# Performance work log

Measured on AMD Instinct MI355X. Metric: run time of the kernel, lower is better.

Reference implementation:

```python
import jax, jax.numpy as jnp
import numpy as np

PATCHES = [(4, 4), (2, 2)]  # (width, height) per stream chunk
SCALE = 2
DM = 256


def conv2d(x, w, bias, pad=0):
    y = jax.lax.conv_general_dilated(
        x, w, window_strides=(1, 1), padding=[(pad, pad), (pad, pad)],
        dimension_numbers=("NCHW", "OIHW", "NCHW"))
    return y + bias[None, :, None, None]


def to_patches(x, b, t, dk, out_h, ph, out_w, pw):
    # x: [b*t, dk, out_h*ph, out_w*pw] -> [b, t*out_h*out_w, dk*ph*pw]
    x = x.reshape(b, t, dk, out_h, ph, out_w, pw)
    return x.transpose(0, 1, 3, 5, 2, 4, 6).reshape(b, t * out_h * out_w, dk * ph * pw)


def from_patches(y, b, t, dk, out_h, ph, out_w, pw):
    # y: [b, t*out_h*out_w, dk*ph*pw] -> [b*t, dk, out_h*ph, out_w*pw]
    y = y.reshape(b, t, out_h, out_w, dk, ph, pw)
    return y.transpose(0, 1, 4, 2, 5, 3, 6).reshape(b * t, dk, out_h * ph, out_w * pw)


def attention(q, k, v):
    d = q.shape[-1]
    scores = jnp.einsum("bnd,bmd->bnm", q, k) / jnp.sqrt(jnp.asarray(d, q.dtype))
    p = jax.nn.softmax(scores, axis=-1)
    return jnp.einsum("bnm,bmd->bnd", p, v)


def forward(x_lo, x_hi, b,
            wq_lo, bq_lo, wk_lo, bk_lo, wv_lo, bv_lo,
            wq_hi, bq_hi, wk_hi, bk_hi, wv_hi, bv_hi,
            wo_lo, bo_lo, wo_hi, bo_hi):
    bt_lo, _, h, w = x_lo.shape
    bt_hi, _, h_, w_ = x_hi.shape
    t_lo = bt_lo // b
    t_hi = bt_hi // b
    n_p = len(PATCHES)
    d_k_lo = DM * SCALE ** 2 // n_p
    d_k_hi = DM // n_p

    q_lo_all = conv2d(x_lo, wq_lo, bq_lo)
    k_lo_all = conv2d(x_lo, wk_lo, bk_lo)
    v_lo_all = conv2d(x_lo, wv_lo, bv_lo)
    q_hi_all = conv2d(x_hi, wq_hi, bq_hi)
    k_hi_all = conv2d(x_hi, wk_hi, bk_hi)
    v_hi_all = conv2d(x_hi, wv_hi, bv_hi)

    outs_lo, outs_hi = [], []
    for i, (width, height) in enumerate(PATCHES):
        out_w, out_h = w // width, h // height
        sl_lo = slice(i * d_k_lo, (i + 1) * d_k_lo)
        sl_hi = slice(i * d_k_hi, (i + 1) * d_k_hi)
        ql = to_patches(q_lo_all[:, sl_lo], b, t_lo, d_k_lo, out_h, height, out_w, width)
        kl = to_patches(k_lo_all[:, sl_lo], b, t_lo, d_k_lo, out_h, height, out_w, width)
        vl = to_patches(v_lo_all[:, sl_lo], b, t_lo, d_k_lo, out_h, height, out_w, width)
        qh = to_patches(q_hi_all[:, sl_hi], b, t_hi, d_k_hi, out_h, height * SCALE, out_w, width * SCALE)
        kh = to_patches(k_hi_all[:, sl_hi], b, t_hi, d_k_hi, out_h, height * SCALE, out_w, width * SCALE)
        vh = to_patches(v_hi_all[:, sl_hi], b, t_hi, d_k_hi, out_h, height * SCALE, out_w, width * SCALE)

        q = jnp.concatenate([ql, qh], axis=1)
        k = jnp.concatenate([kl, kh], axis=1)
        v = jnp.concatenate([vl, vh], axis=1)
        y = attention(q, k, v)

        n_lo = t_lo * out_h * out_w
        y_lo = from_patches(y[:, :n_lo], b, t_lo, d_k_lo, out_h, height, out_w, width)
        y_hi = from_patches(y[:, n_lo:], b, t_hi, d_k_hi, out_h, height * SCALE, out_w, width * SCALE)
        outs_lo.append(y_lo)
        outs_hi.append(y_hi)

    out_lo = jnp.concatenate(outs_lo, axis=1)
    out_hi = jnp.concatenate(outs_hi, axis=1)
    out_lo = jax.nn.leaky_relu(conv2d(out_lo, wo_lo, bo_lo, pad=1), 0.2)
    out_hi = jax.nn.leaky_relu(conv2d(out_hi, wo_hi, bo_hi, pad=1), 0.2)
    return out_lo, out_hi


def setup_inputs() -> dict:
    key = jax.random.key(0)
    ks = jax.random.split(key, 12)
    dm2 = DM * SCALE ** 2  # 1024
    s = 0.02
    inp = {
        "x_lo": jax.random.normal(ks[0], (16, DM, 32, 32), jnp.float32),
        "x_hi": jax.random.normal(ks[1], (16, DM, 64, 64), jnp.float32),
        "b": 4,
        "wq_lo": jax.random.normal(ks[2], (dm2, DM, 1, 1), jnp.float32) * s,
        "bq_lo": jnp.zeros((dm2,), jnp.float32),
        "wk_lo": jax.random.normal(ks[3], (dm2, DM, 1, 1), jnp.float32) * s,
        "bk_lo": jnp.zeros((dm2,), jnp.float32),
        "wv_lo": jax.random.normal(ks[4], (dm2, DM, 1, 1), jnp.float32) * s,
        "bv_lo": jnp.zeros((dm2,), jnp.float32),
        "wq_hi": jax.random.normal(ks[5], (DM, DM, 1, 1), jnp.float32) * s,
        "bq_hi": jnp.zeros((DM,), jnp.float32),
        "wk_hi": jax.random.normal(ks[6], (DM, DM, 1, 1), jnp.float32) * s,
        "bk_hi": jnp.zeros((DM,), jnp.float32),
        "wv_hi": jax.random.normal(ks[7], (DM, DM, 1, 1), jnp.float32) * s,
        "bv_hi": jnp.zeros((DM,), jnp.float32),
        "wo_lo": jax.random.normal(ks[8], (DM, dm2, 3, 3), jnp.float32) * s,
        "bo_lo": jnp.zeros((DM,), jnp.float32),
        "wo_hi": jax.random.normal(ks[9], (DM, DM, 3, 3), jnp.float32) * s,
        "bo_hi": jnp.zeros((DM,), jnp.float32),
    }
    return inp


def reference(x_lo, x_hi, b,
              wq_lo, bq_lo, wk_lo, bk_lo, wv_lo, bv_lo,
              wq_hi, bq_hi, wk_hi, bk_hi, wv_hi, bv_hi,
              wo_lo, bo_lo, wo_hi, bo_hi):
    return forward(x_lo, x_hi, b,
                   wq_lo, bq_lo, wk_lo, bk_lo, wv_lo, bv_lo,
                   wq_hi, bq_hi, wk_hi, bk_hi, wv_hi, bv_hi,
                   wo_lo, bo_lo, wo_hi, bo_hi)
```

## Files before the change

kernel.cpp:

```cpp
#include <hip/hip_runtime.h>
#include <hip/hip_bf16.h>
#include <stdint.h>

typedef __attribute__((ext_vector_type(8))) short short8;
typedef __attribute__((ext_vector_type(4))) short short4v;
typedef __attribute__((ext_vector_type(2))) short short2v;
typedef __attribute__((ext_vector_type(4))) float floatx4;

__device__ __forceinline__ unsigned short f2b(float f) {
  unsigned u = __builtin_bit_cast(unsigned, f);
  unsigned r = u + 0x7fffu + ((u >> 16) & 1u);
  return (unsigned short)(r >> 16);
}
__device__ __forceinline__ float b2f(unsigned short h) {
  unsigned u = ((unsigned)h) << 16;
  return __builtin_bit_cast(float, u);
}
__device__ __forceinline__ void glds16(const unsigned short* src, unsigned short* dst) {
  __builtin_amdgcn_global_load_lds((const __attribute__((address_space(1))) void*)src,
                                   (__attribute__((address_space(3))) void*)dst, 16, 0, 0);
}
__device__ __forceinline__ int swz(int r, int o) {
  return (r << 9) + (o ^ ((((o >> 7) & 3) ^ (r & 7)) << 4));
}

struct GemmP {
  const unsigned short* A;
  const unsigned short* B;
  long sAb, sBb;
  int lda, ldb, K;
  unsigned short* C; long sCb; int ldc;
  float* Cp;
  const float* bias;
  unsigned short *Q0, *K0, *V0t, *Q1, *K1, *V1t;
};

template<int EPI>
__global__ __launch_bounds__(512) void gemm256(GemmP p) {
  __shared__ __align__(16) unsigned short LDS[65536];
  const int tid = threadIdx.x;
  const int wv = tid >> 6, lane = tid & 63;
  const int wm = wv >> 2, wn = wv & 3;
  const int g = lane >> 4, l16 = lane & 15;
  const int bz = blockIdx.z;
  const int m0 = blockIdx.y * 256, n0 = blockIdx.x * 256;

  int bb = bz, koff = 0, Keff = p.K;
  if constexpr (EPI == 1) { bb = bz >> 3; koff = (bz & 7) * (p.K >> 3); Keff = p.K >> 3; }
  const unsigned short* Ab = p.A + (long)bb * p.sAb + (long)m0 * p.lda + koff;
  const unsigned short* Bb = p.B + (long)bb * p.sBb + (long)n0 * p.ldb + koff;
  const int NT = Keff >> 5;

  const int r0 = tid >> 2;
  const int cs = (tid & 3) ^ ((r0 >> 1) & 3);
  const unsigned short* aS0 = Ab + (long)r0 * p.lda + cs * 8;
  const unsigned short* aS1 = aS0 + (long)128 * p.lda;
  const unsigned short* bS0 = Bb + (long)r0 * p.ldb + cs * 8;
  const unsigned short* bS1 = bS0 + (long)128 * p.ldb;
  unsigned short* const lds0 = (unsigned short*)LDS;
  const int wbase = wv * 512;

  auto STAGE_A = [&](int t) {
    unsigned short* d = lds0 + (t & 3) * 16384;
    const long ko = (long)t * 32;
    glds16(aS0 + ko, d + wbase);
    glds16(aS1 + ko, d + 4096 + wbase);
  };
  auto STAGE_B = [&](int t) {
    unsigned short* d = lds0 + (t & 3) * 16384 + 8192;
    const long ko = (long)t * 32;
    glds16(bS0 + ko, d + wbase);
    glds16(bS1 + ko, d + 4096 + wbase);
  };

  STAGE_A(0); STAGE_B(0); STAGE_A(1); STAGE_B(1); STAGE_A(2); STAGE_B(2);

  floatx4 acc[8][4];
  const floatx4 z4 = {0.f, 0.f, 0.f, 0.f};
#pragma unroll
  for (int i = 0; i < 8; ++i)
#pragma unroll
    for (int j = 0; j < 4; ++j) acc[i][j] = z4;

  const int loff = l16 * 32 + ((g ^ ((l16 >> 1) & 3)) * 8);
  const int aRowB = wm * 128;

  for (int t = 0; t < NT; ++t) {
    const unsigned short* As = lds0 + (t & 3) * 16384;
    const unsigned short* Bs = As + 8192;
    if (t < NT - 2)        asm volatile("s_waitcnt vmcnt(8)" ::: "memory");
    else if (t == NT - 2)  asm volatile("s_waitcnt vmcnt(4)" ::: "memory");
    else                   asm volatile("s_waitcnt vmcnt(0)" ::: "memory");
    __builtin_amdgcn_s_barrier();
    __builtin_amdgcn_sched_barrier(0);
    if (t + 3 < NT) STAGE_A(t + 3);
    short8 bf[4], af[4], ag[4];
#pragma unroll
    for (int ni = 0; ni < 4; ++ni)
      bf[ni] = *(const short8*)(Bs + (wn * 64 + ni * 16) * 32 + loff);
#pragma unroll
    for (int mi = 0; mi < 4; ++mi)
      af[mi] = *(const short8*)(As + (aRowB + mi * 16) * 32 + loff);
#pragma unroll
    for (int mi = 0; mi < 4; ++mi)
      ag[mi] = *(const short8*)(As + (aRowB + 64 + mi * 16) * 32 + loff);
    __builtin_amdgcn_s_setprio(1);
#pragma unroll
    for (int mi = 0; mi < 4; ++mi)
#pragma unroll
      for (int ni = 0; ni < 4; ++ni)
        acc[mi][ni] = __builtin_amdgcn_mfma_f32_16x16x32_bf16(af[mi], bf[ni], acc[mi][ni], 0, 0, 0);
    __builtin_amdgcn_s_setprio(0);
    if (t + 3 < NT) STAGE_B(t + 3);
    __builtin_amdgcn_s_setprio(1);
#pragma unroll
    for (int mi = 0; mi < 4; ++mi)
#pragma unroll
      for (int ni = 0; ni < 4; ++ni)
        acc[4 + mi][ni] = __builtin_amdgcn_mfma_f32_16x16x32_bf16(ag[mi], bf[ni], acc[4 + mi][ni], 0, 0, 0);
    __builtin_amdgcn_s_setprio(0);
  }

  if constexpr (EPI == 1) {
    float* C = p.Cp + (long)bz * p.sCb;
#pragma unroll
    for (int mi = 0; mi < 8; ++mi) {
#pragma unroll
      for (int ni = 0; ni < 4; ++ni) {
        const int col = n0 + wn * 64 + ni * 16 + l16;
#pragma unroll
        for (int r4 = 0; r4 < 4; ++r4) {
          const int row = m0 + wm * 128 + mi * 16 + g * 4 + r4;
          C[(long)row * p.ldc + col] = acc[mi][ni][r4];
        }
      }
    }
  } else {
    __syncthreads();
    char* shb = (char*)LDS;
    const int sel = (EPI == 2) ? (m0 >> 10) : (m0 >> 8);
#pragma unroll
    for (int mi = 0; mi < 8; ++mi) {
#pragma unroll
      for (int ni = 0; ni < 4; ++ni) {
        const int c = wn * 64 + ni * 16 + l16;
#pragma unroll
        for (int r4 = 0; r4 < 4; ++r4) {
          const int rr = wm * 128 + mi * 16 + g * 4 + r4;
          float v = acc[mi][ni][r4];
          if constexpr (EPI == 2 || EPI == 3) {
            v += p.bias[m0 + rr];
            if (sel == 0) {
              float sc;
              if constexpr (EPI == 2) sc = ((m0 & 1023) < 512) ? 0.011048543456039806f
                                                               : 0.02209708691207961f;
              else                    sc = (rr < 128) ? 0.011048543456039806f
                                                      : 0.02209708691207961f;
              v *= sc;
            }
          }
          *(unsigned short*)(shb + swz(rr, c * 2)) = f2b(v);
        }
      }
    }
    __syncthreads();

    if constexpr (EPI == 0) {
      unsigned short* C = p.C + (long)bz * p.sCb;
#pragma unroll
      for (int j = 0; j < 16; ++j) {
        const int e = j * 512 + tid;
        const int r = e >> 5, ck = e & 31;
        short8 v = *(const short8*)(shb + swz(r, ck * 16));
        *(short8*)(C + (long)(m0 + r) * p.ldc + n0 + ck * 8) = v;
      }
    } else if constexpr (EPI == 2) {
      const int chb = m0 & 1023;
      const bool cfg0 = chb < 512;
      const int b = bz >> 2, tt = bz & 3;
      const int k0 = n0 >> 8;
      unsigned short* dst = cfg0 ? (sel == 0 ? p.Q0 : sel == 1 ? p.K0 : p.V0t)
                                 : (sel == 0 ? p.Q1 : sel == 1 ? p.K1 : p.V1t);
      if (sel != 2) {
        if (cfg0) {
          const long base = (long)(b * 512) * 8192;
#pragma unroll
          for (int j = 0; j < 16; ++j) {
            const int e = j * 512 + tid;
            const int pi = e >> 9, idx2 = e & 511;
            const int ch = idx2 >> 1, hf = idx2 & 1;
            const int oyL = pi >> 3, ox = pi & 7;
            const int nseq = (tt * 8 + 2 * k0 + oyL) * 8 + ox;
            const int yl = oyL * 4 + hf * 2;
            short4v a = *(const short4v*)(shb + swz(ch, (yl * 32 + ox * 4) * 2));
            short4v b2 = *(const short4v*)(shb + swz(ch, ((yl + 1) * 32 + ox * 4) * 2));
            short8 v = {a[0], a[1], a[2], a[3], b2[0], b2[1], b2[2], b2[3]};
            *(short8*)(dst + base + (long)nseq * 8192 + (chb + ch) * 16 + hf * 8) = v;
          }
        } else {
          const int c2lo = chb - 512;
          const long base = (long)(b * 2048) * 2048;
#pragma unroll
          for (int j = 0; j < 16; ++j) {
            const int e = j * 512 + tid;
            const int pi = e >> 7, cp = e & 127;
            const int oyL = pi >> 4, ox = pi & 15;
            const int nseq = (tt * 16 + 4 * k0 + oyL) * 16 + ox;
            short8 v;
#pragma unroll
            for (int rr = 0; rr < 2; ++rr) {
#pragma unroll
              for (int k = 0; k < 2; ++k) {
                short2v pr = *(const short2v*)(shb +
                    swz(cp * 2 + rr, ((oyL * 2 + k) * 32 + ox * 2) * 2));
                v[rr * 4 + k * 2] = pr[0];
                v[rr * 4 + k * 2 + 1] = pr[1];
              }
            }
            *(short8*)(dst + base + (long)nseq * 2048 + (c2lo + cp * 2) * 4) = v;
          }
        }
      } else {
        if (cfg0) {
          const long base = (long)(b * 8192) * 512;
#pragma unroll
          for (int j = 0; j < 16; ++j) {
            const int e = j * 512 + tid;
            const int oyL = e >> 12, fu = e & 4095;
            const int ch = fu >> 4, pp = fu & 15;
            const int py = pp >> 2, px = pp & 3;
            const int yl = oyL * 4 + py;
            short8 v;
#pragma unroll
            for (int ox = 0; ox < 8; ++ox)
              v[ox] = *(const unsigned short*)(shb + swz(ch, (yl * 32 + ox * 4 + px) * 2));
            const long f = (long)(chb + ch) * 16 + pp;
            *(short8*)(dst + base + f * 512 + (tt * 8 + 2 * k0 + oyL) * 8) = v;
          }
        } else {
          const int c2lo = chb - 512;
          const long base = (long)(b * 2048) * 2048;
#pragma unroll
          for (int j = 0; j < 16; ++j) {
            const int e = j * 512 + tid;
            const int he = e & 1, oyL = (e >> 1) & 3, fu = e >> 3;
            const int c2 = fu >> 2, pp = fu & 3;
            const int py = pp >> 1, px = pp & 1;
            const int yl = oyL * 2 + py;
            short8 v;
#pragma unroll
            for (int i = 0; i < 8; ++i) {
              const int ox = he * 8 + i;
              v[i] = *(const unsigned short*)(shb + swz(c2, (yl * 32 + ox * 2 + px) * 2));
            }
            const long f = (long)(c2lo + c2) * 4 + pp;
            *(short8*)(dst + base + f * 2048 + (tt * 16 + 4 * k0 + oyL) * 16 + he * 8) = v;
          }
        }
      }
    } else if constexpr (EPI == 3) {
      const int b = bz >> 2, tt = bz & 3;
      const int k0 = n0 >> 8;
      const int oyA = k0 >> 1, pyb = (k0 & 1) * 4;
      unsigned short* dstA = sel == 0 ? p.Q0 : sel == 1 ? p.K0 : p.V0t;
      unsigned short* dstB = sel == 0 ? p.Q1 : sel == 1 ? p.K1 : p.V1t;
      if (sel != 2) {
#pragma unroll
        for (int j = 0; j < 16; ++j) {
          const int e = j * 512 + tid;
          if (e < 4096) {
            const int ox = e >> 9, cy = e & 511;
            const int ch = cy >> 2, yl = cy & 3;
            const int nseq = 256 + (tt * 8 + oyA) * 8 + ox;
            short8 v = *(const short8*)(shb + swz(ch, (yl * 64 + ox * 8) * 2));
            *(short8*)(dstA + ((long)(b * 512 + nseq)) * 8192 + ch * 64 + (pyb + yl) * 8) = v;
          } else {
            const int ee = e - 4096;
            const int ox = ee >> 8, cc = ee & 255;
            const int c2 = cc >> 1, hf = cc & 1;
            const int nseq = 1024 + (tt * 16 + k0) * 16 + ox;
            short8 v;
#pragma unroll
            for (int k = 0; k < 2; ++k) {
              short4v a = *(const short4v*)(shb +
                  swz(128 + c2, ((hf * 2 + k) * 64 + ox * 4) * 2));
              v[k * 4] = a[0]; v[k * 4 + 1] = a[1]; v[k * 4 + 2] = a[2]; v[k * 4 + 3] = a[3];
            }
            *(short8*)(dstB + ((long)(b * 2048 + nseq)) * 2048 + c2 * 16 + hf * 8) = v;
          }
        }
      } else {
#pragma unroll
        for (int j = 0; j < 16; ++j) {
          const int e = j * 512 + tid;
          if (e < 4096) {
            const int ch = e >> 5, yl = (e >> 3) & 3, px = e & 7;
            short8 v;
#pragma unroll
            for (int ox = 0; ox < 8; ++ox)
              v[ox] = *(const unsigned short*)(shb + swz(ch, (yl * 64 + ox * 8 + px) * 2));
            const long f = (long)ch * 64 + (pyb + yl) * 8 + px;
            *(short8*)(dstA + ((long)b * 8192 + f) * 512 + 256 + (tt * 8 + oyA) * 8) = v;
          } else {
            const int ee = e - 4096;
            const int he = ee & 1, fu = ee >> 1;
            const int c2 = fu >> 4, pp = fu & 15;
            const int py = pp >> 2, px = pp & 3;
            short8 v;
#pragma unroll
            for (int i = 0; i < 8; ++i) {
              const int x = (he * 8 + i) * 4 + px;
              v[i] = *(const unsigned short*)(shb + swz(128 + c2, (py * 64 + x) * 2));
            }
            const long f = (long)c2 * 16 + pp;
            *(short8*)(dstB + ((long)b * 2048 + f) * 2048 + 1024 + (tt * 16 + k0) * 16 + he * 8) = v;
          }
        }
      }
    }
  }
}

template<int H, int W, int CIN, int KS, bool PARTIAL>
__global__ __launch_bounds__(512) void conv256(const unsigned short* __restrict__ Cinp,
                                               const unsigned short* __restrict__ Wt,
                                               const float* __restrict__ bias,
                                               float* __restrict__ out,
                                               float* __restrict__ P0,
                                               float* __restrict__ P1) {
  constexpr int HP = H + 2, WP = W + 2;
  constexpr int CC = CIN / KS;
  constexpr int NT = 9 * CC / 32;
  __shared__ __align__(16) unsigned short LDS[65536];
  const int tid = threadIdx.x;
  const int wv = tid >> 6, lane = tid & 63;
  const int wm = wv >> 2, wn = wv & 3;
  const int g = lane >> 4, l16 = lane & 15;
  const int bz = blockIdx.z;
  const int bt = bz / KS, ks = bz % KS;
  const int n0 = blockIdx.x * 256;

  const int r0 = tid >> 2;
  const int cs = (tid & 3) ^ ((r0 >> 1) & 3);
  const unsigned short* wA0 = Wt + (long)r0 * CIN + ks * CC + cs * 8;
  const unsigned short* wA1 = wA0 + (long)128 * CIN;
  const int p0 = n0 + r0, p1 = p0 + 128;
  const int y0p = p0 / W, x0p = p0 % W;
  const int y1p = p1 / W, x1p = p1 % W;
  const unsigned short* cB = Cinp + (long)bt * HP * WP * CIN + ks * CC + cs * 8;
  const unsigned short* pB0 = cB + ((long)y0p * WP + x0p) * CIN;
  const unsigned short* pB1 = cB + ((long)y1p * WP + x1p) * CIN;
  unsigned short* const lds0 = (unsigned short*)LDS;
  const int wbase = wv * 512;

  auto STAGE_A = [&](int t) {
    unsigned short* d = lds0 + (t & 3) * 16384;
    const int tap = t >> 3, tc = (t & 7) * 32;
    const long off = (long)tap * (256L * CIN) + tc;
    glds16(wA0 + off, d + wbase);
    glds16(wA1 + off, d + 4096 + wbase);
  };
  auto STAGE_B = [&](int t) {
    unsigned short* d = lds0 + (t & 3) * 16384 + 8192;
    const int tap = t >> 3, tc = (t & 7) * 32;
    const int ky = tap / 3, kx = tap - ky * 3;
    const long off = ((long)ky * WP + kx) * CIN + tc;
    glds16(pB0 + off, d + wbase);
    glds16(pB1 + off, d + 4096 + wbase);
  };

  STAGE_A(0); STAGE_B(0); STAGE_A(1); STAGE_B(1); STAGE_A(2); STAGE_B(2);

  floatx4 acc[8][4];
  const floatx4 z4 = {0.f, 0.f, 0.f, 0.f};
#pragma unroll
  for (int i = 0; i < 8; ++i)
#pragma unroll
    for (int j = 0; j < 4; ++j) acc[i][j] = z4;

  const int loff = l16 * 32 + ((g ^ ((l16 >> 1) & 3)) * 8);
  const int aRowB = wm * 128;

  for (int t = 0; t < NT; ++t) {
    const unsigned short* As = lds0 + (t & 3) * 16384;
    const unsigned short* Bs = As + 8192;
    if (t < NT - 2)        asm volatile("s_waitcnt vmcnt(8)" ::: "memory");
    else if (t == NT - 2)  asm volatile("s_waitcnt vmcnt(4)" ::: "memory");
    else                   asm volatile("s_waitcnt vmcnt(0)" ::: "memory");
    __builtin_amdgcn_s_barrier();
    __builtin_amdgcn_sched_barrier(0);
    if (t + 3 < NT) STAGE_A(t + 3);
    short8 bf[4], af[4], ag[4];
#pragma unroll
    for (int ni = 0; ni < 4; ++ni)
      bf[ni] = *(const short8*)(Bs + (wn * 64 + ni * 16) * 32 + loff);
#pragma unroll
    for (int mi = 0; mi < 4; ++mi)
      af[mi] = *(const short8*)(As + (aRowB + mi * 16) * 32 + loff);
#pragma unroll
    for (int mi = 0; mi < 4; ++mi)
      ag[mi] = *(const short8*)(As + (aRowB + 64 + mi * 16) * 32 + loff);
    __builtin_amdgcn_s_setprio(1);
#pragma unroll
    for (int mi = 0; mi < 4; ++mi)
#pragma unroll
      for (int ni = 0; ni < 4; ++ni)
        acc[mi][ni] = __builtin_amdgcn_mfma_f32_16x16x32_bf16(af[mi], bf[ni], acc[mi][ni], 0, 0, 0);
    __builtin_amdgcn_s_setprio(0);
    if (t + 3 < NT) STAGE_B(t + 3);
    __builtin_amdgcn_s_setprio(1);
#pragma unroll
    for (int mi = 0; mi < 4; ++mi)
#pragma unroll
      for (int ni = 0; ni < 4; ++ni)
        acc[4 + mi][ni] = __builtin_amdgcn_mfma_f32_16x16x32_bf16(ag[mi], bf[ni], acc[4 + mi][ni], 0, 0, 0);
    __builtin_amdgcn_s_setprio(0);
  }

  if constexpr (!PARTIAL) {
#pragma unroll
    for (int mi = 0; mi < 8; ++mi) {
#pragma unroll
      for (int ni = 0; ni < 4; ++ni) {
        const int pn = n0 + wn * 64 + ni * 16 + l16;
        const int y = pn / W, x = pn % W;
#pragma unroll
        for (int r4 = 0; r4 < 4; ++r4) {
          const int co = wm * 128 + mi * 16 + g * 4 + r4;
          float v = acc[mi][ni][r4] + bias[co];
          v = v > 0.f ? v : 0.2f * v;
          out[(((long)bt * 256 + co) * H + y) * W + x] = v;
        }
      }
    }
  } else {
    float* pout = (ks < 2 ? P0 : P1) + (long)(ks & 1) * (16L * 256 * H * W);
#pragma unroll
    for (int mi = 0; mi < 8; ++mi) {
#pragma unroll
      for (int ni = 0; ni < 4; ++ni) {
        const int pn = n0 + wn * 64 + ni * 16 + l16;
        const int y = pn / W, x = pn % W;
#pragma unroll
        for (int r4 = 0; r4 < 4; ++r4) {
          const int co = wm * 128 + mi * 16 + g * 4 + r4;
          pout[(((long)bt * 256 + co) * H + y) * W + x] = acc[mi][ni][r4];
        }
      }
    }
  }
}

template<int L>
__global__ __launch_bounds__(256) void softmax_rows(unsigned short* S) {
  const int w = threadIdx.x >> 6, lane = threadIdx.x & 63;
  const long row = (long)blockIdx.x * 4 + w;
  unsigned short* R = S + row * L;
  constexpr int NC = L / 64;
  float v[NC];
  float m = -1e30f;
#pragma unroll
  for (int i = 0; i < NC; ++i) { v[i] = b2f(R[i * 64 + lane]); m = fmaxf(m, v[i]); }
#pragma unroll
  for (int off = 32; off; off >>= 1) m = fmaxf(m, __shfl_xor(m, off, 64));
  float s = 0.f;
#pragma unroll
  for (int i = 0; i < NC; ++i) { v[i] = __expf(v[i] - m); s += v[i]; }
#pragma unroll
  for (int off = 32; off; off >>= 1) s += __shfl_xor(s, off, 64);
  const float inv = 1.0f / s;
#pragma unroll
  for (int i = 0; i < NC; ++i) R[i * 64 + lane] = f2b(v[i] * inv);
}

__global__ __launch_bounds__(256) void softmax_red8(const float* __restrict__ P,
                                                    unsigned short* __restrict__ S) {
  const int w = threadIdx.x >> 6, lane = threadIdx.x & 63;
  const int rowg = blockIdx.x * 4 + w;
  const int b = rowg >> 9, n = rowg & 511;
  const float* base = P + ((long)b * 8) * 262144 + (long)n * 512 + lane;
  float v[8];
#pragma unroll
  for (int i = 0; i < 8; ++i) {
    float s = 0.f;
#pragma unroll
    for (int ks = 0; ks < 8; ++ks) s += base[(long)ks * 262144 + i * 64];
    v[i] = s;
  }
  float m = -1e30f;
#pragma unroll
  for (int i = 0; i < 8; ++i) m = fmaxf(m, v[i]);
#pragma unroll
  for (int off = 32; off; off >>= 1) m = fmaxf(m, __shfl_xor(m, off, 64));
  float s = 0.f;
#pragma unroll
  for (int i = 0; i < 8; ++i) { v[i] = __expf(v[i] - m); s += v[i]; }
#pragma unroll
  for (int off = 32; off; off >>= 1) s += __shfl_xor(s, off, 64);
  const float inv = 1.0f / s;
  unsigned short* R = S + (long)rowg * 512;
#pragma unroll
  for (int i = 0; i < 8; ++i) R[i * 64 + lane] = f2b(v[i] * inv);
}

__global__ __launch_bounds__(256) void xt_kernel(const float* __restrict__ x,
                                                 unsigned short* __restrict__ xt, int NPIX) {
  __shared__ unsigned short tile[64 * 65];
  const int tid = threadIdx.x;
  const int bt = blockIdx.z, ch0 = blockIdx.y * 64;
  const long pix0 = (long)blockIdx.x * 64;
  const float* src = x + ((long)bt * 256 + ch0) * NPIX + pix0;
#pragma unroll
  for (int i = 0; i < 16; ++i) {
    const int lin = i * 256 + tid;
    const int ch = lin >> 6, px = lin & 63;
    tile[ch * 65 + px] = f2b(src[(long)ch * NPIX + px]);
  }
  __syncthreads();
  unsigned short* dst = xt + ((long)bt * NPIX + pix0) * 256 + ch0;
#pragma unroll
  for (int i = 0; i < 16; ++i) {
    const int lin = i * 256 + tid;
    const int px = lin >> 6, ch = lin & 63;
    dst[(long)px * 256 + ch] = tile[ch * 65 + px];
  }
}

__global__ void prep_qkv_w(const float* wq, const float* wk, const float* wv,
                           const float* bq, const float* bk, const float* bv,
                           unsigned short* Wcat, float* Bcat, int CO) {
  const int idx = blockIdx.x * 256 + threadIdx.x;
  const int n = 3 * CO * 256;
  if (idx < n) {
    const int sel = idx / (CO * 256);
    const int r = idx - sel * CO * 256;
    const float* wsel = sel == 0 ? wq : (sel == 1 ? wk : wv);
    Wcat[idx] = f2b(wsel[r]);
  }
  if (idx < 3 * CO) {
    const int sel = idx / CO;
    const int r = idx - sel * CO;
    const float* bsel = sel == 0 ? bq : (sel == 1 ? bk : bv);
    Bcat[idx] = bsel[r];
  }
}

__global__ void prep_conv_w(const float* wo, unsigned short* Wt, int CIN) {
  const int idx = blockIdx.x * 256 + threadIdx.x;
  const int n = 9 * 256 * CIN;
  if (idx < n) {
    const int t9 = idx / (256 * CIN);
    const int rem = idx - t9 * 256 * CIN;
    const int o = rem / CIN, i = rem - o * CIN;
    Wt[idx] = f2b(wo[((long)o * CIN + i) * 9 + t9]);
  }
}

__global__ __launch_bounds__(256) void zero_border(unsigned short* buf, int HP, int WP, int C) {
  const long i = (long)blockIdx.x * 256 + threadIdx.x;
  const int per_px = C >> 3;
  const int strip = 2 * WP + 2 * (HP - 2);
  const long tot = (long)16 * strip * per_px;
  if (i >= tot) return;
  const int c8 = (int)(i % per_px);
  const long r = i / per_px;
  const int s = (int)(r % strip);
  const int bt = (int)(r / strip);
  int y, x;
  if (s < WP) { y = 0; x = s; }
  else if (s < 2 * WP) { y = HP - 1; x = s - WP; }
  else if (s < 2 * WP + (HP - 2)) { y = s - 2 * WP + 1; x = 0; }
  else { y = s - 2 * WP - (HP - 2) + 1; x = WP - 1; }
  const short8 z = {0, 0, 0, 0, 0, 0, 0, 0};
  *(short8*)(buf + (((long)bt * HP + y) * WP + x) * C + c8 * 8) = z;
}

__global__ __launch_bounds__(256) void repack_lo(const unsigned short* __restrict__ Y0,
                                                 const unsigned short* __restrict__ Y1,
                                                 unsigned short* __restrict__ out) {
  const int tid = threadIdx.x;
  const int blk = blockIdx.x;
  if (blk < 1024) {
    const int b = blk >> 8, n = blk & 255;
    const int t = n >> 6, oh = (n >> 3) & 7, ow = n & 7;
    const unsigned short* row = Y0 + ((long)(b * 512 + n)) * 8192;
    const int bt = b * 4 + t;
#pragma unroll
    for (int j = 0; j < 32; ++j) {
      const int idx = j * 256 + tid;
      const int pp = idx >> 9, ch = idx & 511;
      const int py = pp >> 2, px = pp & 3;
      out[(((long)bt * 34 + oh * 4 + py + 1) * 34 + ow * 4 + px + 1) * 1024 + ch] = row[ch * 16 + pp];
    }
  } else {
    const int q = blk - 1024;
    const int b = q >> 10, n = q & 1023;
    const int t = n >> 8, oh = (n >> 4) & 15, ow = n & 15;
    const unsigned short* row = Y1 + ((long)(b * 2048 + n)) * 2048;
    const int bt = b * 4 + t;
#pragma unroll
    for (int j = 0; j < 8; ++j) {
      const int idx = j * 256 + tid;
      const int pp = idx >> 9, ch = idx & 511;
      const int py = pp >> 1, px = pp & 1;
      out[(((long)bt * 34 + oh * 2 + py + 1) * 34 + ow * 2 + px + 1) * 1024 + 512 + ch] = row[ch * 4 + pp];
    }
  }
}

__global__ __launch_bounds__(256) void repack_hi(const unsigned short* __restrict__ Y0,
                                                 const unsigned short* __restrict__ Y1,
                                                 unsigned short* __restrict__ out) {
  const int tid = threadIdx.x;
  const int blk = blockIdx.x;
  if (blk < 1024) {
    const int b = blk >> 8, n = blk & 255;
    const int t = n >> 6, oh = (n >> 3) & 7, ow = n & 7;
    const unsigned short* row = Y0 + ((long)(b * 512 + 256 + n)) * 8192;
    const int bt = b * 4 + t;
#pragma unroll
    for (int j = 0; j < 32; ++j) {
      const int idx = j * 256 + tid;
      const int pp = idx >> 7, ch = idx & 127;
      const int py = pp >> 3, px = pp & 7;
      out[(((long)bt * 66 + oh * 8 + py + 1) * 66 + ow * 8 + px + 1) * 256 + ch] = row[ch * 64 + pp];
    }
  } else {
    const int q = blk - 1024;
    const int b = q >> 10, n = q & 1023;
    const int t = n >> 8, oh = (n >> 4) & 15, ow = n & 15;
    const unsigned short* row = Y1 + ((long)(b * 2048 + 1024 + n)) * 2048;
    const int bt = b * 4 + t;
#pragma unroll
    for (int j = 0; j < 8; ++j) {
      const int idx = j * 256 + tid;
      const int pp = idx >> 7, ch = idx & 127;
      const int py = pp >> 2, px = pp & 3;
      out[(((long)bt * 66 + oh * 4 + py + 1) * 66 + ow * 4 + px + 1) * 256 + 128 + ch] = row[ch * 16 + pp];
    }
  }
}

__global__ __launch_bounds__(256) void reduce_lrelu(const floatx4* __restrict__ P0,
                                                    const floatx4* __restrict__ P1,
                                                    const float* __restrict__ bias,
                                                    floatx4* __restrict__ out) {
  const long i = (long)blockIdx.x * 256 + threadIdx.x;
  constexpr long SL = 1048576;
  floatx4 a = P0[i], b = P0[SL + i], c = P1[i], d = P1[SL + i];
  const int co = ((int)(i >> 8)) & 255;
  const float bv = bias[co];
  floatx4 r;
#pragma unroll
  for (int j = 0; j < 4; ++j) {
    float v = a[j] + b[j] + c[j] + d[j] + bv;
    r[j] = v > 0.f ? v : 0.2f * v;
  }
  out[i] = r;
}

extern "C" void kernel_launch(void* const* d_in, const int* in_sizes, int n_in,
                              void* d_out, int out_size, void* d_ws, size_t ws_size,
                              hipStream_t stream) {
  (void)in_sizes; (void)n_in; (void)out_size; (void)ws_size;
  const float* x_lo = (const float*)d_in[0];
  const float* x_hi = (const float*)d_in[1];
  const float* wq_lo = (const float*)d_in[3];
  const float* bq_lo = (const float*)d_in[4];
  const float* wk_lo = (const float*)d_in[5];
  const float* bk_lo = (const float*)d_in[6];
  const float* wv_lo = (const float*)d_in[7];
  const float* bv_lo = (const float*)d_in[8];
  const float* wq_hi = (const float*)d_in[9];
  const float* bq_hi = (const float*)d_in[10];
  const float* wk_hi = (const float*)d_in[11];
  const float* bk_hi = (const float*)d_in[12];
  const float* wv_hi = (const float*)d_in[13];
  const float* bv_hi = (const float*)d_in[14];
  const float* wo_lo = (const float*)d_in[15];
  const float* bo_lo = (const float*)d_in[16];
  const float* wo_hi = (const float*)d_in[17];
  const float* bo_hi = (const float*)d_in[18];
  float* out = (float*)d_out;

  char* ws = (char*)d_ws;
  const long B0 = 33554432;
  unsigned short* Qp0 = (unsigned short*)(ws);
  unsigned short* Kp0 = (unsigned short*)(ws + B0);
  unsigned short* V0t = (unsigned short*)(ws + 2 * B0);
  unsigned short* Qp1 = (unsigned short*)(ws + 3 * B0);
  unsigned short* Kp1 = (unsigned short*)(ws + 4 * B0);
  unsigned short* V1t = (unsigned short*)(ws + 5 * B0);
  char* ptr = ws + 6 * B0;
  unsigned short* S0 = (unsigned short*)ptr;     ptr += 2097152;
  unsigned short* Xt_lo = (unsigned short*)ptr;  ptr += 8388608;
  unsigned short* Xt_hi = (unsigned short*)ptr;  ptr += 33554432;
  unsigned short* Wcat_lo = (unsigned short*)ptr; ptr += 1572864;
  unsigned short* Wcat_hi = (unsigned short*)ptr; ptr += 393216;
  float* Bcat_lo = (float*)ptr;                  ptr += 12288;
  float* Bcat_hi = (float*)ptr;                  ptr += 3072;
  unsigned short* Wt_lo = (unsigned short*)ptr;  ptr += 4718592;
  unsigned short* Wt_hi = (unsigned short*)ptr;  ptr += 1179648;
  unsigned short* S1 = Kp0;
  unsigned short* Y0 = Qp0;
  unsigned short* Y1 = Qp1;
  unsigned short* CinP_lo = Kp0;
  unsigned short* CinP_hi = Kp1;
  float* S0p = (float*)Xt_hi;
  float* PC0 = (float*)Qp0;
  float* PC1 = (float*)Qp1;

  prep_qkv_w<<<(3 * 1024 * 256 + 255) / 256, 256, 0, stream>>>(
      wq_lo, wk_lo, wv_lo, bq_lo, bk_lo, bv_lo, Wcat_lo, Bcat_lo, 1024);
  prep_qkv_w<<<(3 * 256 * 256 + 255) / 256, 256, 0, stream>>>(
      wq_hi, wk_hi, wv_hi, bq_hi, bk_hi, bv_hi, Wcat_hi, Bcat_hi, 256);
  prep_conv_w<<<(9 * 256 * 1024 + 255) / 256, 256, 0, stream>>>(wo_lo, Wt_lo, 1024);
  prep_conv_w<<<(9 * 256 * 256 + 255) / 256, 256, 0, stream>>>(wo_hi, Wt_hi, 256);
  xt_kernel<<<dim3(16, 4, 16), 256, 0, stream>>>(x_lo, Xt_lo, 1024);
  xt_kernel<<<dim3(64, 4, 16), 256, 0, stream>>>(x_hi, Xt_hi, 4096);

  {
    GemmP p{};
    p.A = Wcat_lo; p.B = Xt_lo; p.sAb = 0; p.sBb = 1024L * 256;
    p.lda = 256; p.ldb = 256; p.K = 256;
    p.bias = Bcat_lo;
    p.Q0 = Qp0; p.K0 = Kp0; p.V0t = V0t; p.Q1 = Qp1; p.K1 = Kp1; p.V1t = V1t;
    gemm256<2><<<dim3(4, 12, 16), 512, 0, stream>>>(p);
    p.A = Wcat_hi; p.B = Xt_hi; p.sBb = 4096L * 256; p.bias = Bcat_hi;
    gemm256<3><<<dim3(16, 3, 16), 512, 0, stream>>>(p);
  }

  {
    GemmP s{};
    s.A = Qp0; s.B = Kp0; s.sAb = 512L * 8192; s.sBb = 512L * 8192;
    s.lda = 8192; s.ldb = 8192; s.K = 8192;
    s.Cp = S0p; s.sCb = 512L * 512; s.ldc = 512;
    gemm256<1><<<dim3(2, 2, 32), 512, 0, stream>>>(s);
    softmax_red8<<<512, 256, 0, stream>>>(S0p, S0);
    GemmP pv{};
    pv.A = S0; pv.B = V0t; pv.sAb = 512L * 512; pv.sBb = 8192L * 512;
    pv.lda = 512; pv.ldb = 512; pv.K = 512;
    pv.C = Y0; pv.sCb = 512L * 8192; pv.ldc = 8192;
    gemm256<0><<<dim3(32, 2, 4), 512, 0, stream>>>(pv);
  }

  {
    GemmP s{};
    s.A = Qp1; s.B = Kp1; s.sAb = 2048L * 2048; s.sBb = 2048L * 2048;
    s.lda = 2048; s.ldb = 2048; s.K = 2048;
    s.C = S1; s.sCb = 2048L * 2048; s.ldc = 2048;
    gemm256<0><<<dim3(8, 8, 4), 512, 0, stream>>>(s);
    softmax_rows<2048><<<2048, 256, 0, stream>>>(S1);
    GemmP pv{};
    pv.A = S1; pv.B = V1t; pv.sAb = 2048L * 2048; pv.sBb = 2048L * 2048;
    pv.lda = 2048; pv.ldb = 2048; pv.K = 2048;
    pv.C = Y1; pv.sCb = 2048L * 2048; pv.ldc = 2048;
    gemm256<0><<<dim3(8, 8, 4), 512, 0, stream>>>(pv);
  }

  zero_border<<<1056, 256, 0, stream>>>(CinP_lo, 34, 34, 1024);
  zero_border<<<520, 256, 0, stream>>>(CinP_hi, 66, 66, 256);
  repack_lo<<<5120, 256, 0, stream>>>(Y0, Y1, CinP_lo);
  repack_hi<<<5120, 256, 0, stream>>>(Y0, Y1, CinP_hi);

  conv256<32, 32, 1024, 4, true><<<dim3(4, 1, 64), 512, 0, stream>>>(
      CinP_lo, Wt_lo, bo_lo, out, PC0, PC1);
  reduce_lrelu<<<4096, 256, 0, stream>>>((const floatx4*)PC0, (const floatx4*)PC1, bo_lo,
                                         (floatx4*)out);
  conv256<64, 64, 256, 1, false><<<dim3(16, 1, 16), 512, 0, stream>>>(
      CinP_hi, Wt_hi, bo_hi, out + 4194304, nullptr, nullptr);
}
```

Baseline: 613.9 us.

## Split-K sixteen-way for patch scores with bf16 partials; LDS-transposed repacks

The split-K for the lo-stream score GEMM goes from 8 to 16 slices, which doubles the grid, and the partial sums are now stored as bf16 instead of fp32. The softmax reduction kernel is changed to sum 16 bf16 partials. The repack kernels are reorganised by source buffer: each block reads one contiguous row, transposes it through LDS, and writes 16-byte vectors. This replaces the old strided scalar gathers and scatters. Rounding partial sums to bf16 lowers the precision of the attention scores.

```diff
diff --git a/kernel.cpp b/kernel.cpp
--- a/kernel.cpp
+++ b/kernel.cpp
@@ -30,7 +30,6 @@
   long sAb, sBb;
   int lda, ldb, K;
   unsigned short* C; long sCb; int ldc;
-  float* Cp;
   const float* bias;
   unsigned short *Q0, *K0, *V0t, *Q1, *K1, *V1t;
 };
@@ -46,7 +45,7 @@
   const int m0 = blockIdx.y * 256, n0 = blockIdx.x * 256;
 
   int bb = bz, koff = 0, Keff = p.K;
-  if constexpr (EPI == 1) { bb = bz >> 3; koff = (bz & 7) * (p.K >> 3); Keff = p.K >> 3; }
+  if constexpr (EPI == 1) { bb = bz >> 4; koff = (bz & 15) * (p.K >> 4); Keff = p.K >> 4; }
   const unsigned short* Ab = p.A + (long)bb * p.sAb + (long)m0 * p.lda + koff;
   const unsigned short* Bb = p.B + (long)bb * p.sBb + (long)n0 * p.ldb + koff;
   const int NT = Keff >> 5;
@@ -122,7 +121,7 @@
   }
 
   if constexpr (EPI == 1) {
-    float* C = p.Cp + (long)bz * p.sCb;
+    unsigned short* C = p.C + (long)bz * p.sCb;
 #pragma unroll
     for (int mi = 0; mi < 8; ++mi) {
 #pragma unroll
@@ -131,7 +130,7 @@
 #pragma unroll
         for (int r4 = 0; r4 < 4; ++r4) {
           const int row = m0 + wm * 128 + mi * 16 + g * 4 + r4;
-          C[(long)row * p.ldc + col] = acc[mi][ni][r4];
+          C[(long)row * p.ldc + col] = f2b(acc[mi][ni][r4]);
         }
       }
     }
@@ -473,18 +472,18 @@
   for (int i = 0; i < NC; ++i) R[i * 64 + lane] = f2b(v[i] * inv);
 }
 
-__global__ __launch_bounds__(256) void softmax_red8(const float* __restrict__ P,
-                                                    unsigned short* __restrict__ S) {
+__global__ __launch_bounds__(256) void softmax_red16(const unsigned short* __restrict__ P,
+                                                     unsigned short* __restrict__ S) {
   const int w = threadIdx.x >> 6, lane = threadIdx.x & 63;
   const int rowg = blockIdx.x * 4 + w;
   const int b = rowg >> 9, n = rowg & 511;
-  const float* base = P + ((long)b * 8) * 262144 + (long)n * 512 + lane;
+  const unsigned short* base = P + ((long)b * 16) * 262144 + (long)n * 512 + lane;
   float v[8];
 #pragma unroll
   for (int i = 0; i < 8; ++i) {
     float s = 0.f;
 #pragma unroll
-    for (int ks = 0; ks < 8; ++ks) s += base[(long)ks * 262144 + i * 64];
+    for (int ks = 0; ks < 16; ++ks) s += b2f(base[(long)ks * 262144 + i * 64]);
     v[i] = s;
   }
   float m = -1e30f;
@@ -575,69 +574,98 @@
   *(short8*)(buf + (((long)bt * HP + y) * WP + x) * C + c8 * 8) = z;
 }
 
-__global__ __launch_bounds__(256) void repack_lo(const unsigned short* __restrict__ Y0,
-                                                 const unsigned short* __restrict__ Y1,
-                                                 unsigned short* __restrict__ out) {
+__global__ __launch_bounds__(256) void repackY0(const unsigned short* __restrict__ Y0,
+                                                unsigned short* __restrict__ CinLo,
+                                                unsigned short* __restrict__ CinHi) {
+  __shared__ __align__(16) unsigned short T[8704];
+  const int r = blockIdx.x;
+  const int b = r >> 9, n = r & 511;
   const int tid = threadIdx.x;
-  const int blk = blockIdx.x;
-  if (blk < 1024) {
-    const int b = blk >> 8, n = blk & 255;
+  const int wv2 = tid >> 6, lane = tid & 63;
+  const unsigned short* row = Y0 + (long)r * 8192;
+  if (n < 256) {
+#pragma unroll
+    for (int q = 0; q < 4; ++q) {
+      short8 v = *(const short8*)(row + tid * 32 + q * 8);
+#pragma unroll
+      for (int j = 0; j < 8; ++j) {
+        const int f = tid * 32 + q * 8 + j;
+        T[(f & 15) * 520 + (f >> 4)] = (unsigned short)v[j];
+      }
+    }
+    __syncthreads();
     const int t = n >> 6, oh = (n >> 3) & 7, ow = n & 7;
-    const unsigned short* row = Y0 + ((long)(b * 512 + n)) * 8192;
     const int bt = b * 4 + t;
 #pragma unroll
-    for (int j = 0; j < 32; ++j) {
-      const int idx = j * 256 + tid;
-      const int pp = idx >> 9, ch = idx & 511;
+    for (int it = 0; it < 4; ++it) {
+      const int pp = it * 4 + wv2;
       const int py = pp >> 2, px = pp & 3;
-      out[(((long)bt * 34 + oh * 4 + py + 1) * 34 + ow * 4 + px + 1) * 1024 + ch] = row[ch * 16 + pp];
+      short8 v = *(const short8*)(T + pp * 520 + lane * 8);
+      *(short8*)(CinLo + (((long)bt * 34 + oh * 4 + py + 1) * 34 + ow * 4 + px + 1) * 1024
+                 + lane * 8) = v;
     }
   } else {
-    const int q = blk - 1024;
-    const int b = q >> 10, n = q & 1023;
+    const int m = n - 256;
+#pragma unroll
+    for (int q = 0; q < 4; ++q) {
+      short8 v = *(const short8*)(row + tid * 32 + q * 8);
+#pragma unroll
+      for (int j = 0; j < 8; ++j) {
+        const int f = tid * 32 + q * 8 + j;
+        T[(f & 63) * 136 + (f >> 6)] = (unsigned short)v[j];
+      }
+    }
+    __syncthreads();
+    const int t = m >> 6, oh = (m >> 3) & 7, ow = m & 7;
+    const int bt = b * 4 + t;
+#pragma unroll
+    for (int it = 0; it < 4; ++it) {
+      const int pp = it * 16 + wv2 * 4 + (lane >> 4);
+      const int py = pp >> 3, px = pp & 7;
+      short8 v = *(const short8*)(T + pp * 136 + (lane & 15) * 8);
+      *(short8*)(CinHi + (((long)bt * 66 + oh * 8 + py + 1) * 66 + ow * 8 + px + 1) * 256
+                 + (lane & 15) * 8) = v;
+    }
+  }
+}
+
+__global__ __launch_bounds__(256) void repackY1(const unsigned short* __restrict__ Y1,
+                                                unsigned short* __restrict__ CinLo,
+                                                unsigned short* __restrict__ CinHi) {
+  __shared__ __align__(16) unsigned short T[2176];
+  const int r = blockIdx.x;
+  const int b = r >> 11, n = r & 2047;
+  const int tid = threadIdx.x;
+  const int wv2 = tid >> 6, lane = tid & 63;
+  const unsigned short* row = Y1 + (long)r * 2048;
+  short8 v = *(const short8*)(row + tid * 8);
+  if (n < 1024) {
+#pragma unroll
+    for (int j = 0; j < 8; ++j) {
+      const int f = tid * 8 + j;
+      T[(f & 3) * 520 + (f >> 2)] = (unsigned short)v[j];
+    }
+    __syncthreads();
     const int t = n >> 8, oh = (n >> 4) & 15, ow = n & 15;
-    const unsigned short* row = Y1 + ((long)(b * 2048 + n)) * 2048;
     const int bt = b * 4 + t;
+    const int pp = wv2, py = pp >> 1, px = pp & 1;
+    short8 o = *(const short8*)(T + pp * 520 + lane * 8);
+    *(short8*)(CinLo + (((long)bt * 34 + oh * 2 + py + 1) * 34 + ow * 2 + px + 1) * 1024
+               + 512 + lane * 8) = o;
+  } else {
+    const int m = n - 1024;
 #pragma unroll
     for (int j = 0; j < 8; ++j) {
-      const int idx = j * 256 + tid;
-      const int pp = idx >> 9, ch = idx & 511;
-      const int py = pp >> 1, px = pp & 1;
-      out[(((long)bt * 34 + oh * 2 + py + 1) * 34 + ow * 2 + px + 1) * 1024 + 512 + ch] = row[ch * 4 + pp];
-    }
-  }
-}
-
-__global__ __launch_bounds__(256) void repack_hi(const unsigned short* __restrict__ Y0,
-                                                 const unsigned short* __restrict__ Y1,
-                                                 unsigned short* __restrict__ out) {
-  const int tid = threadIdx.x;
-  const int blk = blockIdx.x;
-  if (blk < 1024) {
-    const int b = blk >> 8, n = blk & 255;
-    const int t = n >> 6, oh = (n >> 3) & 7, ow = n & 7;
-    const unsigned short* row = Y0 + ((long)(b * 512 + 256 + n)) * 8192;
+      const int f = tid * 8 + j;
+      T[(f & 15) * 136 + (f >> 4)] = (unsigned short)v[j];
+    }
+    __syncthreads();
+    const int t = m >> 8, oh = (m >> 4) & 15, ow = m & 15;
     const int bt = b * 4 + t;
-#pragma unroll
-    for (int j = 0; j < 32; ++j) {
-      const int idx = j * 256 + tid;
-      const int pp = idx >> 7, ch = idx & 127;
-      const int py = pp >> 3, px = pp & 7;
-      out[(((long)bt * 66 + oh * 8 + py + 1) * 66 + ow * 8 + px + 1) * 256 + ch] = row[ch * 64 + pp];
-    }
-  } else {
-    const int q = blk - 1024;
-    const int b = q >> 10, n = q & 1023;
-    const int t = n >> 8, oh = (n >> 4) & 15, ow = n & 15;
-    const unsigned short* row = Y1 + ((long)(b * 2048 + 1024 + n)) * 2048;
-    const int bt = b * 4 + t;
-#pragma unroll
-    for (int j = 0; j < 8; ++j) {
-      const int idx = j * 256 + tid;
-      const int pp = idx >> 7, ch = idx & 127;
-      const int py = pp >> 2, px = pp & 3;
-      out[(((long)bt * 66 + oh * 4 + py + 1) * 66 + ow * 4 + px + 1) * 256 + 128 + ch] = row[ch * 16 + pp];
-    }
+    const int pp = wv2 * 4 + (lane >> 4), py = pp >> 2, px = pp & 3;
+    short8 o = *(const short8*)(T + pp * 136 + (lane & 15) * 8);
+    *(short8*)(CinHi + (((long)bt * 66 + oh * 4 + py + 1) * 66 + ow * 4 + px + 1) * 256
+               + 128 + (lane & 15) * 8) = o;
   }
 }
 
@@ -706,7 +734,7 @@
   unsigned short* Y1 = Qp1;
   unsigned short* CinP_lo = Kp0;
   unsigned short* CinP_hi = Kp1;
-  float* S0p = (float*)Xt_hi;
+  unsigned short* S0p = Xt_hi;
   float* PC0 = (float*)Qp0;
   float* PC1 = (float*)Qp1;
 
@@ -734,9 +762,9 @@
     GemmP s{};
     s.A = Qp0; s.B = Kp0; s.sAb = 512L * 8192; s.sBb = 512L * 8192;
     s.lda = 8192; s.ldb = 8192; s.K = 8192;
-    s.Cp = S0p; s.sCb = 512L * 512; s.ldc = 512;
-    gemm256<1><<<dim3(2, 2, 32), 512, 0, stream>>>(s);
-    softmax_red8<<<512, 256, 0, stream>>>(S0p, S0);
+    s.C = S0p; s.sCb = 262144; s.ldc = 512;
+    gemm256<1><<<dim3(2, 2, 64), 512, 0, stream>>>(s);
+    softmax_red16<<<512, 256, 0, stream>>>(S0p, S0);
     GemmP pv{};
     pv.A = S0; pv.B = V0t; pv.sAb = 512L * 512; pv.sBb = 8192L * 512;
     pv.lda = 512; pv.ldb = 512; pv.K = 512;
@@ -760,8 +788,8 @@
 
   zero_border<<<1056, 256, 0, stream>>>(CinP_lo, 34, 34, 1024);
   zero_border<<<520, 256, 0, stream>>>(CinP_hi, 66, 66, 256);
-  repack_lo<<<5120, 256, 0, stream>>>(Y0, Y1, CinP_lo);
-  repack_hi<<<5120, 256, 0, stream>>>(Y0, Y1, CinP_hi);
+  repackY0<<<2048, 256, 0, stream>>>(Y0, CinP_lo, CinP_hi);
+  repackY1<<<8192, 256, 0, stream>>>(Y1, CinP_lo, CinP_hi);
 
   conv256<32, 32, 1024, 4, true><<<dim3(4, 1, 64), 512, 0, stream>>>(
       CinP_lo, Wt_lo, bo_lo, out, PC0, PC1);
```

Measured after the change: 580.5 us. 1.06x faster.
